# Performance work log

Hardware: AMD Instinct MI355X
Metric: run time of the kernel (lower is better)

The kernel has to match this reference:

```python
import jax, jax.numpy as jnp
import numpy as np

N, E, S, G = 20000, 60000, 3000, 128
EAD = 5
DIMS = [(16, 32), (32, 64), (64, 64)]  # NNConv (M_in, M_out) per layer
HID = 128  # edge-MLP hidden
FC_IN = 64 + 8  # conv output + raw continuous feats


def setup_inputs() -> dict:
    key = jax.random.key(0)
    ks = iter(jax.random.split(key, 64))
    inp = {}
    inp['x'] = jax.random.normal(next(ks), (N, 24), jnp.float32)
    inp['edge_index'] = jax.random.randint(next(ks), (2, E), 0, N)
    inp['edge_attr'] = jax.random.uniform(next(ks), (E, EAD), jnp.float32)
    inp['node_to_subgraph'] = jnp.sort(jax.random.randint(next(ks), (N,), 0, S))
    inp['subgraph_to_graph'] = jnp.sort(jax.random.randint(next(ks), (S,), 0, G))
    for i, (mi, mo) in enumerate(DIMS):
        inp[f'conv{i}_w1'] = jax.random.normal(next(ks), (EAD, HID), jnp.float32) / np.sqrt(EAD)
        inp[f'conv{i}_b1'] = jnp.zeros((HID,), jnp.float32)
        inp[f'conv{i}_w2'] = jax.random.normal(next(ks), (HID, mi * mo), jnp.float32) / np.sqrt(HID * mi)
        inp[f'conv{i}_b2'] = jnp.zeros((mi * mo,), jnp.float32)
        inp[f'conv{i}_root'] = jax.random.normal(next(ks), (mi, mo), jnp.float32) / np.sqrt(mi)
        inp[f'conv{i}_bias'] = jnp.zeros((mo,), jnp.float32)
    dims_fc = [(FC_IN, FC_IN // 2), (FC_IN // 2, FC_IN // 4), (FC_IN // 4, 1)]
    for i, (di, do) in enumerate(dims_fc):
        inp[f'fc{i+1}_w'] = jax.random.normal(next(ks), (di, do), jnp.float32) / np.sqrt(di)
        inp[f'fc{i+1}_b'] = jnp.zeros((do,), jnp.float32)
    return inp


def _nnconv(x, src, dst, ea, w1, b1, w2, b2, root, bias):
    # edge MLP -> per-edge weight matrix [E, M_in, M_out]
    h = jax.nn.relu(ea @ w1 + b1)
    mi, mo = root.shape
    W = (h @ w2 + b2).reshape(-1, mi, mo)
    msg = jnp.einsum('ei,eio->eo', x[src], W)  # gather + per-edge matmul
    agg = jax.ops.segment_sum(msg, dst, num_segments=x.shape[0])  # scatter-add
    return agg + x @ root + bias


def _mean_pool(x, seg, num):
    s = jax.ops.segment_sum(x, seg, num_segments=num)
    c = jax.ops.segment_sum(jnp.ones((x.shape[0], 1), x.dtype), seg, num_segments=num)
    return s / jnp.maximum(c, 1.0)


def _forward(x, edge_index, edge_attr, node_to_subgraph, subgraph_to_graph, convs, fcs):
    src, dst = edge_index[0], edge_index[1]
    xi = x[:, :16]
    for p in convs:
        xi = jax.nn.elu(_nnconv(xi, src, dst, edge_attr, *p))
    x_cont = x[:, 16:]
    xc = jnp.concatenate([xi, x_cont], axis=1)  # [N, 72]
    xs = _mean_pool(xc, node_to_subgraph, S)    # [S, 72]
    xg = _mean_pool(xs, subgraph_to_graph, G)   # [G, 72]
    (w1, b1), (w2, b2), (w3, b3) = fcs
    xg = jax.nn.elu(xg @ w1 + b1)
    xg = jax.nn.elu(xg @ w2 + b2)
    return (xg @ w3 + b3).reshape(-1)


def reference(x, edge_index, edge_attr, node_to_subgraph, subgraph_to_graph,
              conv0_w1, conv0_b1, conv0_w2, conv0_b2, conv0_root, conv0_bias,
              conv1_w1, conv1_b1, conv1_w2, conv1_b2, conv1_root, conv1_bias,
              conv2_w1, conv2_b1, conv2_w2, conv2_b2, conv2_root, conv2_bias,
              fc1_w, fc1_b, fc2_w, fc2_b, fc3_w, fc3_b):
    convs = [
        (conv0_w1, conv0_b1, conv0_w2, conv0_b2, conv0_root, conv0_bias),
        (conv1_w1, conv1_b1, conv1_w2, conv1_b2, conv1_root, conv1_bias),
        (conv2_w1, conv2_b1, conv2_w2, conv2_b2, conv2_root, conv2_bias),
    ]
    fcs = [(fc1_w, fc1_b), (fc2_w, fc2_b), (fc3_w, fc3_b)]
    return _forward(x, edge_index, edge_attr, node_to_subgraph, subgraph_to_graph, convs, fcs)
```

## Files before the change

### kernel.cpp

```cpp
#include <hip/hip_runtime.h>
#include <hip/hip_bf16.h>
#include <cmath>

#define NN 20000
#define NE 60000
#define NS 3000
#define NG 128
#define HIDN 128
#define SCB 79

typedef float f32x16 __attribute__((ext_vector_type(16)));
typedef _Float16 f16x8 __attribute__((ext_vector_type(8)));

__device__ __forceinline__ float eluf(float v) { return v > 0.f ? v : expm1f(v); }

__device__ __forceinline__ void gload_lds16(const void* g, void* l) {
    __builtin_amdgcn_global_load_lds(
        (const __attribute__((address_space(1))) unsigned int*)g,
        (__attribute__((address_space(3))) unsigned int*)l, 16, 0, 0);
}

__device__ __forceinline__ void vmwait0() {
    asm volatile("s_waitcnt vmcnt(0)" ::: "memory");
}
__device__ __forceinline__ void vmwait8() {
    asm volatile("s_waitcnt vmcnt(8)" ::: "memory");
}

__global__ void k_hist(const int* __restrict__ dst, int* __restrict__ deg) {
    int e = blockIdx.x * 256 + threadIdx.x;
    if (e < NE) atomicAdd(&deg[dst[e]], 1);
}

__global__ void k_scan1(const int* __restrict__ deg, int* __restrict__ bsum) {
    __shared__ int s[256];
    const int t = threadIdx.x;
    int i = blockIdx.x * 256 + t;
    s[t] = (i < NN) ? deg[i] : 0;
    __syncthreads();
#pragma unroll
    for (int off = 128; off > 0; off >>= 1) {
        if (t < off) s[t] += s[t + off];
        __syncthreads();
    }
    if (t == 0) bsum[blockIdx.x] = s[0];
}

__global__ void k_scan2(const int* __restrict__ bsum, int* __restrict__ boff) {
    __shared__ int s[SCB];
    const int t = threadIdx.x;
    if (t < SCB) s[t] = bsum[t];
    __syncthreads();
    if (t == 0) {
        int acc = 0;
        for (int i = 0; i < SCB; ++i) { int v = s[i]; s[i] = acc; acc += v; }
    }
    __syncthreads();
    if (t < SCB) boff[t] = s[t];
}

__global__ void k_scan3(const int* __restrict__ deg, const int* __restrict__ boff,
                        int* __restrict__ rowptr) {
    __shared__ int s[256];
    const int t = threadIdx.x;
    int i = blockIdx.x * 256 + t;
    int v = (i < NN) ? deg[i] : 0;
    s[t] = v;
    __syncthreads();
#pragma unroll
    for (int off = 1; off < 256; off <<= 1) {
        int a = (t >= off) ? s[t - off] : 0;
        __syncthreads();
        s[t] += a;
        __syncthreads();
    }
    if (i < NN) rowptr[i + 1] = boff[blockIdx.x] + s[t];
    if (i == 0) rowptr[0] = 0;
}

__global__ void k_scatter(const int* __restrict__ src, const int* __restrict__ dst,
                          const int* __restrict__ rowptr, int* __restrict__ tmp,
                          int* __restrict__ eord, int* __restrict__ srcS) {
    int e = blockIdx.x * 256 + threadIdx.x;
    if (e >= NE) return;
    int d = dst[e];
    int pos = rowptr[d] + atomicAdd(&tmp[d], 1);
    eord[pos] = e;
    srcS[pos] = src[e];
}

template <int MI, int MO>
__global__ void k_w2t(const float* __restrict__ w2, const float* __restrict__ b2,
                      _Float16* __restrict__ w2t) {
    constexpr int KP = 129 * MI;
    constexpr int KF = 128 * MI;
    int idx = blockIdx.x * 256 + threadIdx.x;
    if (idx >= MO * KP) return;
    int o = idx / KP, kg = idx % KP;
    float v = (kg < KF) ? w2[(size_t)kg * MO + o] : b2[(kg - KF) * MO + o];
    w2t[idx] = (_Float16)v;
}

__global__ void k_x16h(const float* __restrict__ x, _Float16* __restrict__ xh) {
    int idx = blockIdx.x * 256 + threadIdx.x;
    if (idx >= NN * 16) return;
    int n = idx >> 4, i = idx & 15;
    xh[idx] = (_Float16)x[n * 24 + i];
}

template <int MI, int MO, int XS>
__global__ __launch_bounds__(256, 2) void k_edgeB(
    const _Float16* __restrict__ xi, const float* __restrict__ ea,
    const float* __restrict__ w1, const float* __restrict__ b1,
    const _Float16* __restrict__ w2t, const int* __restrict__ srcS,
    const int* __restrict__ eord, float* __restrict__ msg) {
    constexpr int PH  = MI / 16;
    constexpr int KP  = 129 * MI;
    constexpr int NT  = MO / 32;
    constexpr int CH  = 16 / (PH * NT);
    constexpr int NCH = 64 / CH;
    static_assert(CH * PH * NT == 16, "ITEMS must be 16");
    static_assert(NCH % 2 == 0, "chunk loop unrolled x2");

    __shared__ __align__(16) _Float16 sb[2][2][16 * 512];

    const int lane = threadIdx.x & 63;
    const int w    = threadIdx.x >> 6;
    const int mg   = w & 1;
    const int kh   = w >> 1;
    const int lo5  = lane & 31;
    const int hi   = lane >> 5;
    const int e0   = blockIdx.x * 128 + mg * 64;
    const int kb   = kh * 64;

    const int rc0 = min(e0 + lo5, NE - 1);
    const int rc1 = min(e0 + 32 + lo5, NE - 1);
    const int s0 = srcS[rc0];
    const int s1 = srcS[rc1];

    float ea0[5], ea1[5];
    {
        const int eo0 = eord[rc0], eo1 = eord[rc1];
#pragma unroll
        for (int d = 0; d < 5; ++d) {
            ea0[d] = ea[eo0 * 5 + d];
            ea1[d] = ea[eo1 * 5 + d];
        }
    }

    f16x8 xr0[PH], xr1[PH];
    {
        const _Float16* xb0 = xi + (size_t)s0 * XS + hi * 8;
        const _Float16* xb1 = xi + (size_t)s1 * XS + hi * 8;
#pragma unroll
        for (int p = 0; p < PH; ++p) {
            xr0[p] = *reinterpret_cast<const f16x8*>(xb0 + p * 16);
            xr1[p] = *reinterpret_cast<const f16x8*>(xb1 + p * 16);
        }
    }

    f32x16 acc[2][NT];
#pragma unroll
    for (int m = 0; m < 2; ++m)
#pragma unroll
        for (int n = 0; n < NT; ++n)
#pragma unroll
            for (int i = 0; i < 16; ++i) acc[m][n][i] = 0.f;

    auto stage = [&](int buf, int kc) {
#pragma unroll
        for (int jj = 0; jj < 8; ++jj) {
            const int j  = mg + jj * 2;
            const int n  = j % NT;
            const int kp = j / NT;
            const int p  = kp % PH;
            const int kk = kp / PH;
            gload_lds16(w2t + (size_t)(n * 32 + lo5) * KP
                            + (size_t)(kb + kc + kk) * MI + p * 16 + hi * 8,
                        &sb[kh][buf][j * 512]);
        }
    };

    auto calc_h = [&](int kc, _Float16* h0, _Float16* h1) {
#pragma unroll
        for (int kk = 0; kk < CH; ++kk) {
            const int k = kb + kc + kk;
            const float c0 = w1[0 * HIDN + k], c1 = w1[1 * HIDN + k],
                        c2 = w1[2 * HIDN + k], c3 = w1[3 * HIDN + k],
                        c4 = w1[4 * HIDN + k], bb = b1[k];
            float t0 = bb, t1 = bb;
            t0 = fmaf(ea0[0], c0, t0); t1 = fmaf(ea1[0], c0, t1);
            t0 = fmaf(ea0[1], c1, t0); t1 = fmaf(ea1[1], c1, t1);
            t0 = fmaf(ea0[2], c2, t0); t1 = fmaf(ea1[2], c2, t1);
            t0 = fmaf(ea0[3], c3, t0); t1 = fmaf(ea1[3], c3, t1);
            t0 = fmaf(ea0[4], c4, t0); t1 = fmaf(ea1[4], c4, t1);
            h0[kk] = (_Float16)fmaxf(t0, 0.f);
            h1[kk] = (_Float16)fmaxf(t1, 0.f);
        }
    };

    auto compute = [&](int buf, const _Float16* h0, const _Float16* h1) {
        const _Float16* sbc = &sb[kh][buf][0];
#pragma unroll
        for (int kk = 0; kk < CH; ++kk) {
            const _Float16 hv0 = h0[kk];
            const _Float16 hv1 = h1[kk];
            const f16x8 h80 = {hv0, hv0, hv0, hv0, hv0, hv0, hv0, hv0};
            const f16x8 h81 = {hv1, hv1, hv1, hv1, hv1, hv1, hv1, hv1};
#pragma unroll
            for (int p = 0; p < PH; ++p) {
                const f16x8 af0 = xr0[p] * h80;
                const f16x8 af1 = xr1[p] * h81;
#pragma unroll
                for (int n = 0; n < NT; ++n) {
                    const f16x8 bv = *reinterpret_cast<const f16x8*>(
                        &sbc[((kk * PH + p) * NT + n) * 512 + lane * 8]);
                    acc[0][n] = __builtin_amdgcn_mfma_f32_32x32x16_f16(af0, bv, acc[0][n], 0, 0, 0);
                    acc[1][n] = __builtin_amdgcn_mfma_f32_32x32x16_f16(af1, bv, acc[1][n], 0, 0, 0);
                }
            }
        }
    };

    _Float16 hA0[CH], hA1[CH], hB0[CH], hB1[CH];

    stage(0, 0);
    calc_h(0, hA0, hA1);

    for (int c = 0; c < NCH; c += 2) {
        stage(1, (c + 1) * CH);
        calc_h((c + 1) * CH, hB0, hB1);
        vmwait8();
        __builtin_amdgcn_sched_barrier(0);
        __builtin_amdgcn_s_barrier();
        __builtin_amdgcn_sched_barrier(0);
        __builtin_amdgcn_s_setprio(1);
        compute(0, hA0, hA1);
        __builtin_amdgcn_s_setprio(0);
        __builtin_amdgcn_sched_barrier(0);
        __builtin_amdgcn_s_barrier();

        const bool pf = (c + 2 < NCH);
        if (pf) {
            stage(0, (c + 2) * CH);
            calc_h((c + 2) * CH, hA0, hA1);
            vmwait8();
        } else {
            vmwait0();
        }
        __builtin_amdgcn_sched_barrier(0);
        __builtin_amdgcn_s_barrier();
        __builtin_amdgcn_sched_barrier(0);
        __builtin_amdgcn_s_setprio(1);
        compute(1, hB0, hB1);
        __builtin_amdgcn_s_setprio(0);
        __builtin_amdgcn_sched_barrier(0);
        __builtin_amdgcn_s_barrier();
    }

    if (kh == 1) {
#pragma unroll
        for (int p = 0; p < PH; ++p) {
#pragma unroll
            for (int n = 0; n < NT; ++n) {
                const f16x8 bv = *reinterpret_cast<const f16x8*>(
                    w2t + (size_t)(n * 32 + lo5) * KP + (size_t)128 * MI + p * 16 + hi * 8);
                acc[0][n] = __builtin_amdgcn_mfma_f32_32x32x16_f16(xr0[p], bv, acc[0][n], 0, 0, 0);
                acc[1][n] = __builtin_amdgcn_mfma_f32_32x32x16_f16(xr1[p], bv, acc[1][n], 0, 0, 0);
            }
        }
    }

    __syncthreads();
    float* red = reinterpret_cast<float*>(&sb[0][0][0]);
    if (kh == 1) {
#pragma unroll
        for (int m = 0; m < 2; ++m)
#pragma unroll
            for (int n = 0; n < NT; ++n) {
                float* d = red + (size_t)((mg * 2 + m) * NT + n) * 1024 + lane;
#pragma unroll
                for (int i = 0; i < 16; ++i) d[i * 64] = acc[m][n][i];
            }
    }
    __syncthreads();
    if (kh == 0) {
#pragma unroll
        for (int m = 0; m < 2; ++m)
#pragma unroll
            for (int n = 0; n < NT; ++n) {
                const float* s = red + (size_t)((mg * 2 + m) * NT + n) * 1024 + lane;
#pragma unroll
                for (int i = 0; i < 16; ++i) acc[m][n][i] += s[i * 64];
            }
#pragma unroll
        for (int m = 0; m < 2; ++m)
#pragma unroll
            for (int q = 0; q < 4; ++q)
#pragma unroll
                for (int a2 = 0; a2 < 4; ++a2) {
                    const int e = e0 + m * 32 + 4 * hi + 8 * q + a2;
                    if (e < NE) {
#pragma unroll
                        for (int n = 0; n < NT; ++n)
                            msg[(size_t)e * MO + n * 32 + lo5] = acc[m][n][4 * q + a2];
                    }
                }
    }
}

template <int MI, int MO, int XS>
__global__ void k_agg(const float* __restrict__ msg, const int* __restrict__ rowptr,
                      const float* __restrict__ xi, const float* __restrict__ root,
                      const float* __restrict__ bias, float* __restrict__ out,
                      _Float16* __restrict__ outh) {
    int idx = blockIdx.x * 256 + threadIdx.x;
    if (idx >= NN * MO) return;
    int n = idx / MO, o = idx % MO;
    float s = bias[o];
#pragma unroll
    for (int i = 0; i < MI; ++i) s = fmaf(xi[(size_t)n * XS + i], root[i * MO + o], s);
    const int j0 = rowptr[n], j1 = rowptr[n + 1];
    for (int j = j0; j < j1; ++j) s += msg[(size_t)j * MO + o];
    float r = eluf(s);
    out[idx] = r;
    outh[idx] = (_Float16)r;
}

__global__ void k_pool_s(const float* __restrict__ xi, const float* __restrict__ x,
                         const int* __restrict__ n2s, float* __restrict__ xs_sum,
                         float* __restrict__ cs) {
    int idx = blockIdx.x * 256 + threadIdx.x;
    if (idx >= NN * 72) return;
    int n = idx / 72, j = idx % 72;
    float v = (j < 64) ? xi[n * 64 + j] : x[n * 24 + 16 + (j - 64)];
    int s = n2s[n];
    atomicAdd(&xs_sum[s * 72 + j], v);
    if (j == 0) atomicAdd(&cs[s], 1.f);
}

__global__ void k_pool_g(const float* __restrict__ xs_sum, const float* __restrict__ cs,
                         const int* __restrict__ s2g, float* __restrict__ xg_sum,
                         float* __restrict__ cg) {
    int idx = blockIdx.x * 256 + threadIdx.x;
    if (idx >= NS * 72) return;
    int s = idx / 72, j = idx % 72;
    float v = xs_sum[s * 72 + j] / fmaxf(cs[s], 1.f);
    int g = s2g[s];
    atomicAdd(&xg_sum[g * 72 + j], v);
    if (j == 0) atomicAdd(&cg[g], 1.f);
}

__global__ void k_fc(const float* __restrict__ xg_sum, const float* __restrict__ cg,
                     const float* __restrict__ w1, const float* __restrict__ b1,
                     const float* __restrict__ w2, const float* __restrict__ b2,
                     const float* __restrict__ w3, const float* __restrict__ b3,
                     float* __restrict__ out) {
    int g = threadIdx.x;
    if (g >= NG) return;
    float inv = 1.f / fmaxf(cg[g], 1.f);
    float v[72];
#pragma unroll
    for (int j = 0; j < 72; ++j) v[j] = xg_sum[g * 72 + j] * inv;
    float h1[36];
#pragma unroll
    for (int o = 0; o < 36; ++o) {
        float s = b1[o];
#pragma unroll
        for (int i = 0; i < 72; ++i) s = fmaf(v[i], w1[i * 36 + o], s);
        h1[o] = eluf(s);
    }
    float h2[18];
#pragma unroll
    for (int o = 0; o < 18; ++o) {
        float s = b2[o];
#pragma unroll
        for (int i = 0; i < 36; ++i) s = fmaf(h1[i], w2[i * 18 + o], s);
        h2[o] = eluf(s);
    }
    float s = b3[0];
#pragma unroll
    for (int i = 0; i < 18; ++i) s = fmaf(h2[i], w3[i], s);
    out[g] = s;
}

extern "C" void kernel_launch(void* const* d_in, const int* in_sizes, int n_in,
                              void* d_out, int out_size, void* d_ws, size_t ws_size,
                              hipStream_t stream) {
    const float* x   = (const float*)d_in[0];
    const int*   ei  = (const int*)d_in[1];
    const float* ea  = (const float*)d_in[2];
    const int*   n2s = (const int*)d_in[3];
    const int*   s2g = (const int*)d_in[4];
    const int* src = ei;
    const int* dst = ei + NE;

    const float* cw1[3]   = {(const float*)d_in[5],  (const float*)d_in[11], (const float*)d_in[17]};
    const float* cb1[3]   = {(const float*)d_in[6],  (const float*)d_in[12], (const float*)d_in[18]};
    const float* cw2[3]   = {(const float*)d_in[7],  (const float*)d_in[13], (const float*)d_in[19]};
    const float* cb2[3]   = {(const float*)d_in[8],  (const float*)d_in[14], (const float*)d_in[20]};
    const float* croot[3] = {(const float*)d_in[9],  (const float*)d_in[15], (const float*)d_in[21]};
    const float* cbias[3] = {(const float*)d_in[10], (const float*)d_in[16], (const float*)d_in[22]};
    const float* fc1w = (const float*)d_in[23];
    const float* fc1b = (const float*)d_in[24];
    const float* fc2w = (const float*)d_in[25];
    const float* fc2b = (const float*)d_in[26];
    const float* fc3w = (const float*)d_in[27];
    const float* fc3b = (const float*)d_in[28];

    char* W = (char*)d_ws;
    float*    xiA   = (float*)(W);
    float*    xiB   = (float*)(W + 5120000);
    _Float16* xiAh  = (_Float16*)(W + 10240000);
    _Float16* xiBh  = (_Float16*)(W + 12800000);
    _Float16* x16h  = (_Float16*)(W + 15360000);
    float*    msg   = (float*)(W + 16000000);
    float*    xs_sum= (float*)(W + 31360000);
    float*    cs    = (float*)(W + 32224000);
    float*    xg_sum= (float*)(W + 32236000);
    float*    cg    = (float*)(W + 32272864);
    _Float16* w2t0  = (_Float16*)(W + 32273376);
    _Float16* w2t1  = (_Float16*)(W + 32405472);
    _Float16* w2t2  = (_Float16*)(W + 32933856);
    int*      deg   = (int*)(W + 33990624);
    int*      tmp   = (int*)(W + 34070624);
    int*      rowptr= (int*)(W + 34150624);
    int*      eord  = (int*)(W + 34230640);
    int*      srcS  = (int*)(W + 34470640);
    int*      bsum  = (int*)(W + 34710640);
    int*      boff  = (int*)(W + 34710960);

    hipMemsetAsync(xs_sum, 0, (size_t)(NS * 72 + NS) * 4 + (size_t)(NG * 72 + NG) * 4, stream);
    hipMemsetAsync(deg, 0, 160000, stream);

    k_hist<<<(NE + 255) / 256, 256, 0, stream>>>(dst, deg);
    k_scan1<<<SCB, 256, 0, stream>>>(deg, bsum);
    k_scan2<<<1, 128, 0, stream>>>(bsum, boff);
    k_scan3<<<SCB, 256, 0, stream>>>(deg, boff, rowptr);
    k_scatter<<<(NE + 255) / 256, 256, 0, stream>>>(src, dst, rowptr, tmp, eord, srcS);

    k_w2t<16, 32><<<(32 * 129 * 16 + 255) / 256, 256, 0, stream>>>(cw2[0], cb2[0], w2t0);
    k_w2t<32, 64><<<(64 * 129 * 32 + 255) / 256, 256, 0, stream>>>(cw2[1], cb2[1], w2t1);
    k_w2t<64, 64><<<(64 * 129 * 64 + 255) / 256, 256, 0, stream>>>(cw2[2], cb2[2], w2t2);
    k_x16h<<<(NN * 16 + 255) / 256, 256, 0, stream>>>(x, x16h);

    const int EB = (NE + 127) / 128;

    k_edgeB<16, 32, 16><<<EB, 256, 0, stream>>>(x16h, ea, cw1[0], cb1[0], w2t0, srcS, eord, msg);
    k_agg<16, 32, 24><<<(NN * 32 + 255) / 256, 256, 0, stream>>>(msg, rowptr, x, croot[0], cbias[0], xiB, xiBh);

    k_edgeB<32, 64, 32><<<EB, 256, 0, stream>>>(xiBh, ea, cw1[1], cb1[1], w2t1, srcS, eord, msg);
    k_agg<32, 64, 32><<<(NN * 64 + 255) / 256, 256, 0, stream>>>(msg, rowptr, xiB, croot[1], cbias[1], xiA, xiAh);

    k_edgeB<64, 64, 64><<<EB, 256, 0, stream>>>(xiAh, ea, cw1[2], cb1[2], w2t2, srcS, eord, msg);
    k_agg<64, 64, 64><<<(NN * 64 + 255) / 256, 256, 0, stream>>>(msg, rowptr, xiA, croot[2], cbias[2], xiB, xiBh);

    k_pool_s<<<(NN * 72 + 255) / 256, 256, 0, stream>>>(xiB, x, n2s, xs_sum, cs);
    k_pool_g<<<(NS * 72 + 255) / 256, 256, 0, stream>>>(xs_sum, cs, s2g, xg_sum, cg);
    k_fc<<<1, 128, 0, stream>>>(xg_sum, cg, fc1w, fc1b, fc2w, fc2b, fc3w, fc3b, (float*)d_out);
}
```

Baseline: 312.7 us.

## Fuse prep kernels, store messages in fp16, fuse last aggregation with pooling

```diff
diff --git a/kernel.cpp b/kernel.cpp
--- a/kernel.cpp
+++ b/kernel.cpp
@@ -89,23 +89,41 @@
     srcS[pos] = src[e];
 }
 
-template <int MI, int MO>
-__global__ void k_w2t(const float* __restrict__ w2, const float* __restrict__ b2,
-                      _Float16* __restrict__ w2t) {
-    constexpr int KP = 129 * MI;
-    constexpr int KF = 128 * MI;
+#define PRE_N0 66048
+#define PRE_N1 264192
+#define PRE_N2 528384
+#define PRE_N3 320000
+#define PRE_TOT (PRE_N0 + PRE_N1 + PRE_N2 + PRE_N3)
+
+__global__ void k_prep(const float* __restrict__ w20, const float* __restrict__ b20,
+                       const float* __restrict__ w21, const float* __restrict__ b21,
+                       const float* __restrict__ w22, const float* __restrict__ b22,
+                       const float* __restrict__ x,
+                       _Float16* __restrict__ w2t0, _Float16* __restrict__ w2t1,
+                       _Float16* __restrict__ w2t2, _Float16* __restrict__ x16h) {
     int idx = blockIdx.x * 256 + threadIdx.x;
-    if (idx >= MO * KP) return;
-    int o = idx / KP, kg = idx % KP;
-    float v = (kg < KF) ? w2[(size_t)kg * MO + o] : b2[(kg - KF) * MO + o];
-    w2t[idx] = (_Float16)v;
-}
-
-__global__ void k_x16h(const float* __restrict__ x, _Float16* __restrict__ xh) {
-    int idx = blockIdx.x * 256 + threadIdx.x;
-    if (idx >= NN * 16) return;
-    int n = idx >> 4, i = idx & 15;
-    xh[idx] = (_Float16)x[n * 24 + i];
+    if (idx < PRE_N0) {
+        constexpr int KP = 129 * 16, KF = 128 * 16, MO = 32;
+        int o = idx / KP, kg = idx % KP;
+        float v = (kg < KF) ? w20[(size_t)kg * MO + o] : b20[(kg - KF) * MO + o];
+        w2t0[idx] = (_Float16)v;
+    } else if (idx < PRE_N0 + PRE_N1) {
+        int i2 = idx - PRE_N0;
+        constexpr int KP = 129 * 32, KF = 128 * 32, MO = 64;
+        int o = i2 / KP, kg = i2 % KP;
+        float v = (kg < KF) ? w21[(size_t)kg * MO + o] : b21[(kg - KF) * MO + o];
+        w2t1[i2] = (_Float16)v;
+    } else if (idx < PRE_N0 + PRE_N1 + PRE_N2) {
+        int i2 = idx - PRE_N0 - PRE_N1;
+        constexpr int KP = 129 * 64, KF = 128 * 64, MO = 64;
+        int o = i2 / KP, kg = i2 % KP;
+        float v = (kg < KF) ? w22[(size_t)kg * MO + o] : b22[(kg - KF) * MO + o];
+        w2t2[i2] = (_Float16)v;
+    } else if (idx < PRE_TOT) {
+        int i2 = idx - PRE_N0 - PRE_N1 - PRE_N2;
+        int n = i2 >> 4, i = i2 & 15;
+        x16h[i2] = (_Float16)x[n * 24 + i];
+    }
 }
 
 template <int MI, int MO, int XS>
@@ -113,7 +131,7 @@
     const _Float16* __restrict__ xi, const float* __restrict__ ea,
     const float* __restrict__ w1, const float* __restrict__ b1,
     const _Float16* __restrict__ w2t, const int* __restrict__ srcS,
-    const int* __restrict__ eord, float* __restrict__ msg) {
+    const int* __restrict__ eord, _Float16* __restrict__ msg) {
     constexpr int PH  = MI / 16;
     constexpr int KP  = 129 * MI;
     constexpr int NT  = MO / 32;
@@ -234,9 +252,7 @@
         __builtin_amdgcn_sched_barrier(0);
         __builtin_amdgcn_s_barrier();
         __builtin_amdgcn_sched_barrier(0);
-        __builtin_amdgcn_s_setprio(1);
         compute(0, hA0, hA1);
-        __builtin_amdgcn_s_setprio(0);
         __builtin_amdgcn_sched_barrier(0);
         __builtin_amdgcn_s_barrier();
 
@@ -251,9 +267,7 @@
         __builtin_amdgcn_sched_barrier(0);
         __builtin_amdgcn_s_barrier();
         __builtin_amdgcn_sched_barrier(0);
-        __builtin_amdgcn_s_setprio(1);
         compute(1, hB0, hB1);
-        __builtin_amdgcn_s_setprio(0);
         __builtin_amdgcn_sched_barrier(0);
         __builtin_amdgcn_s_barrier();
     }
@@ -303,14 +317,15 @@
                     if (e < NE) {
 #pragma unroll
                         for (int n = 0; n < NT; ++n)
-                            msg[(size_t)e * MO + n * 32 + lo5] = acc[m][n][4 * q + a2];
+                            msg[(size_t)e * MO + n * 32 + lo5] =
+                                (_Float16)acc[m][n][4 * q + a2];
                     }
                 }
     }
 }
 
 template <int MI, int MO, int XS>
-__global__ void k_agg(const float* __restrict__ msg, const int* __restrict__ rowptr,
+__global__ void k_agg(const _Float16* __restrict__ msg, const int* __restrict__ rowptr,
                       const float* __restrict__ xi, const float* __restrict__ root,
                       const float* __restrict__ bias, float* __restrict__ out,
                       _Float16* __restrict__ outh) {
@@ -321,22 +336,34 @@
 #pragma unroll
     for (int i = 0; i < MI; ++i) s = fmaf(xi[(size_t)n * XS + i], root[i * MO + o], s);
     const int j0 = rowptr[n], j1 = rowptr[n + 1];
-    for (int j = j0; j < j1; ++j) s += msg[(size_t)j * MO + o];
+    for (int j = j0; j < j1; ++j) s += (float)msg[(size_t)j * MO + o];
     float r = eluf(s);
     out[idx] = r;
     outh[idx] = (_Float16)r;
 }
 
-__global__ void k_pool_s(const float* __restrict__ xi, const float* __restrict__ x,
-                         const int* __restrict__ n2s, float* __restrict__ xs_sum,
-                         float* __restrict__ cs) {
+__global__ void k_agg_pool(const _Float16* __restrict__ msg, const int* __restrict__ rowptr,
+                           const float* __restrict__ xi, const float* __restrict__ root,
+                           const float* __restrict__ bias, const float* __restrict__ x,
+                           const int* __restrict__ n2s, float* __restrict__ xs_sum,
+                           float* __restrict__ cs) {
     int idx = blockIdx.x * 256 + threadIdx.x;
     if (idx >= NN * 72) return;
-    int n = idx / 72, j = idx % 72;
-    float v = (j < 64) ? xi[n * 64 + j] : x[n * 24 + 16 + (j - 64)];
-    int s = n2s[n];
-    atomicAdd(&xs_sum[s * 72 + j], v);
-    if (j == 0) atomicAdd(&cs[s], 1.f);
+    int n = idx / 72, o = idx % 72;
+    float r;
+    if (o < 64) {
+        float s = bias[o];
+#pragma unroll
+        for (int i = 0; i < 64; ++i) s = fmaf(xi[(size_t)n * 64 + i], root[i * 64 + o], s);
+        const int j0 = rowptr[n], j1 = rowptr[n + 1];
+        for (int j = j0; j < j1; ++j) s += (float)msg[(size_t)j * 64 + o];
+        r = eluf(s);
+    } else {
+        r = x[n * 24 + 16 + (o - 64)];
+    }
+    const int sg = n2s[n];
+    atomicAdd(&xs_sum[sg * 72 + o], r);
+    if (o == 0) atomicAdd(&cs[sg], 1.f);
 }
 
 __global__ void k_pool_g(const float* __restrict__ xs_sum, const float* __restrict__ cs,
@@ -414,24 +441,23 @@
     _Float16* xiAh  = (_Float16*)(W + 10240000);
     _Float16* xiBh  = (_Float16*)(W + 12800000);
     _Float16* x16h  = (_Float16*)(W + 15360000);
-    float*    msg   = (float*)(W + 16000000);
-    float*    xs_sum= (float*)(W + 31360000);
-    float*    cs    = (float*)(W + 32224000);
-    float*    xg_sum= (float*)(W + 32236000);
-    float*    cg    = (float*)(W + 32272864);
-    _Float16* w2t0  = (_Float16*)(W + 32273376);
-    _Float16* w2t1  = (_Float16*)(W + 32405472);
-    _Float16* w2t2  = (_Float16*)(W + 32933856);
-    int*      deg   = (int*)(W + 33990624);
-    int*      tmp   = (int*)(W + 34070624);
-    int*      rowptr= (int*)(W + 34150624);
-    int*      eord  = (int*)(W + 34230640);
-    int*      srcS  = (int*)(W + 34470640);
-    int*      bsum  = (int*)(W + 34710640);
-    int*      boff  = (int*)(W + 34710960);
-
-    hipMemsetAsync(xs_sum, 0, (size_t)(NS * 72 + NS) * 4 + (size_t)(NG * 72 + NG) * 4, stream);
-    hipMemsetAsync(deg, 0, 160000, stream);
+    _Float16* msg   = (_Float16*)(W + 16000000);
+    float*    xs_sum= (float*)(W + 23680000);
+    float*    cs    = (float*)(W + 24544000);
+    float*    xg_sum= (float*)(W + 24556000);
+    float*    cg    = (float*)(W + 24592864);
+    int*      deg   = (int*)(W + 24593376);
+    int*      tmp   = (int*)(W + 24673376);
+    _Float16* w2t0  = (_Float16*)(W + 24753376);
+    _Float16* w2t1  = (_Float16*)(W + 24885472);
+    _Float16* w2t2  = (_Float16*)(W + 25413856);
+    int*      rowptr= (int*)(W + 26470624);
+    int*      eord  = (int*)(W + 26550640);
+    int*      srcS  = (int*)(W + 26790640);
+    int*      bsum  = (int*)(W + 27030640);
+    int*      boff  = (int*)(W + 27030960);
+
+    hipMemsetAsync(xs_sum, 0, 1073376, stream);
 
     k_hist<<<(NE + 255) / 256, 256, 0, stream>>>(dst, deg);
     k_scan1<<<SCB, 256, 0, stream>>>(deg, bsum);
@@ -439,10 +465,8 @@
     k_scan3<<<SCB, 256, 0, stream>>>(deg, boff, rowptr);
     k_scatter<<<(NE + 255) / 256, 256, 0, stream>>>(src, dst, rowptr, tmp, eord, srcS);
 
-    k_w2t<16, 32><<<(32 * 129 * 16 + 255) / 256, 256, 0, stream>>>(cw2[0], cb2[0], w2t0);
-    k_w2t<32, 64><<<(64 * 129 * 32 + 255) / 256, 256, 0, stream>>>(cw2[1], cb2[1], w2t1);
-    k_w2t<64, 64><<<(64 * 129 * 64 + 255) / 256, 256, 0, stream>>>(cw2[2], cb2[2], w2t2);
-    k_x16h<<<(NN * 16 + 255) / 256, 256, 0, stream>>>(x, x16h);
+    k_prep<<<(PRE_TOT + 255) / 256, 256, 0, stream>>>(
+        cw2[0], cb2[0], cw2[1], cb2[1], cw2[2], cb2[2], x, w2t0, w2t1, w2t2, x16h);
 
     const int EB = (NE + 127) / 128;
 
@@ -453,9 +477,9 @@
     k_agg<32, 64, 32><<<(NN * 64 + 255) / 256, 256, 0, stream>>>(msg, rowptr, xiB, croot[1], cbias[1], xiA, xiAh);
 
     k_edgeB<64, 64, 64><<<EB, 256, 0, stream>>>(xiAh, ea, cw1[2], cb1[2], w2t2, srcS, eord, msg);
-    k_agg<64, 64, 64><<<(NN * 64 + 255) / 256, 256, 0, stream>>>(msg, rowptr, xiA, croot[2], cbias[2], xiB, xiBh);
-
-    k_pool_s<<<(NN * 72 + 255) / 256, 256, 0, stream>>>(xiB, x, n2s, xs_sum, cs);
+    k_agg_pool<<<(NN * 72 + 255) / 256, 256, 0, stream>>>(msg, rowptr, xiA, croot[2], cbias[2],
+                                                          x, n2s, xs_sum, cs);
+
     k_pool_g<<<(NS * 72 + 255) / 256, 256, 0, stream>>>(xs_sum, cs, s2g, xg_sum, cg);
     k_fc<<<1, 128, 0, stream>>>(xg_sum, cg, fc1w, fc1b, fc2w, fc2b, fc3w, fc3b, (float*)d_out);
 }
```

Measured after the change: 302.0 us. 3.4% less time.
